# Optimization experiments

Hardware: AMD Instinct MI355X
Metric: run time of the kernel (lower is better)

The kernel has to match this reference:

```python
import jax, jax.numpy as jnp
import numpy as np

HIDDEN = 1024
NUM_HEADS = 16
HEAD_DIM = HIDDEN // NUM_HEADS


def setup_inputs() -> dict:
    key = jax.random.key(0)
    ks = jax.random.split(key, 9)
    B, S, Hs = 2, 2048, HIDDEN
    scale = 1.0 / np.sqrt(Hs)
    inp = {
        "hidden_state": jax.random.normal(ks[0], (B, S, Hs), dtype=jnp.float32),
        # causal mask, exactly (B, num_heads, S, S) as the module's assert requires
        "attention_mask": jnp.broadcast_to(
            jnp.tril(jnp.ones((S, S), dtype=bool)), (B, NUM_HEADS, S, S)
        ),
        "wq": jax.random.normal(ks[1], (Hs, Hs), dtype=jnp.float32) * scale,
        "bq": jnp.zeros((Hs,), dtype=jnp.float32),
        "wk": jax.random.normal(ks[2], (Hs, Hs), dtype=jnp.float32) * scale,
        "bk": jnp.zeros((Hs,), dtype=jnp.float32),
        "wv": jax.random.normal(ks[3], (Hs, Hs), dtype=jnp.float32) * scale,
        "bv": jnp.zeros((Hs,), dtype=jnp.float32),
        "wo": jax.random.normal(ks[4], (Hs, Hs), dtype=jnp.float32) * scale,
        "bo": jnp.zeros((Hs,), dtype=jnp.float32),
    }
    return inp


def _split_heads(x):
    B, S, _ = x.shape
    return x.reshape(B, S, NUM_HEADS, HEAD_DIM).transpose(0, 2, 1, 3)  # (B,H,S,D)


def reference(hidden_state, attention_mask, wq, bq, wk, bk, wv, bv, wo, bo):
    B, S, Hs = hidden_state.shape
    # torch nn.Linear: x @ W.T + b
    q = _split_heads(hidden_state @ wq.T + bq)
    k = _split_heads(hidden_state @ wk.T + bk)
    v = _split_heads(hidden_state @ wv.T + bv)
    scores = jnp.einsum("bhsd,bhtd->bhst", q, k) / jnp.sqrt(
        jnp.asarray(HEAD_DIM, dtype=jnp.float32)
    )
    scores = jnp.where(attention_mask, scores, -jnp.inf)
    probs = jax.nn.softmax(scores, axis=-1)
    # dropout p=0.0 (eval/deterministic) -> identity
    out = jnp.einsum("bhst,bhtd->bhsd", probs, v)
    out = out.transpose(0, 2, 1, 3).reshape(B, S, Hs)
    return out @ wo.T + bo
```

## Files before the change

kernel.cpp:

```cpp
#include <hip/hip_runtime.h>
#include <stdint.h>
#include <stddef.h>


typedef __attribute__((ext_vector_type(8))) short short8;
typedef __attribute__((ext_vector_type(4))) float f32x4;
typedef __attribute__((ext_vector_type(4))) unsigned int u32x4;
typedef __attribute__((ext_vector_type(2))) unsigned int u32x2;
typedef __attribute__((ext_vector_type(4))) unsigned short u16x4;

static __device__ __forceinline__ unsigned short f2bf(float f){
  union { float f; unsigned u; } v; v.f = f;
  unsigned r = v.u + 0x7FFFu + ((v.u >> 16) & 1u);
  return (unsigned short)(r >> 16);
}
static __device__ __forceinline__ unsigned pk2bf(float lo, float hi){
  return (unsigned)f2bf(lo) | ((unsigned)f2bf(hi) << 16);
}

static __device__ __forceinline__ void gl_lds16(const void* g, void* l){
  __builtin_amdgcn_global_load_lds((const __attribute__((address_space(1))) void*)g,
                                   (__attribute__((address_space(3))) void*)l, 16, 0, 0);
}

__global__ __launch_bounds__(256) void k_cvt_all(const float* __restrict__ X,
                                                 const float* __restrict__ w0, const float* __restrict__ w1,
                                                 const float* __restrict__ w2, const float* __restrict__ w3,
                                                 unsigned short* __restrict__ Xb,
                                                 unsigned short* __restrict__ Wb){
  int bid = blockIdx.x;
  const float* src; unsigned short* dst; int i;
  if (bid < 4096){ src = X; dst = Xb; i = bid*256 + threadIdx.x; }
  else {
    int w = (bid - 4096) >> 10;
    const float* srcs[4] = {w0,w1,w2,w3};
    src = srcs[w]; dst = Wb + (size_t)w*1048576u;
    i = ((bid - 4096) & 1023)*256 + threadIdx.x;
  }
  f32x4 x = ((const f32x4*)src)[i];
  u16x4 y = { f2bf(x[0]), f2bf(x[1]), f2bf(x[2]), f2bf(x[3]) };
  ((u16x4*)dst)[i] = y;
}

template<int MODE, int MT>
__global__ __launch_bounds__(256) void k_gemm_bt(
    const unsigned short* __restrict__ A,
    const unsigned short* __restrict__ B,
    const float* __restrict__ bias0, const float* __restrict__ bias1, const float* __restrict__ bias2,
    void* __restrict__ Cout, unsigned short* __restrict__ Vt, int N, int K)
{
  static_assert(MT==64 || MT==128, "MT");
  constexpr int I  = MT/32;
  constexpr int NA = MT/64;
  __shared__ unsigned short lds_a[MT*32];
  __shared__ unsigned short lds_b[128*32];
  const int t = threadIdx.x;
  const int lane = t & 63, wave = t >> 6;
  const int wy = wave >> 1, wx = wave & 1;
  const int m0 = blockIdx.y * MT, n0 = blockIdx.x * 128;
  const int mrow = lane & 15, quad = lane >> 4;
  const unsigned short* ga = A + (size_t)(m0 + (t>>2)) * K + (t&3)*8;
  const unsigned short* gb = B + (size_t)(n0 + (t>>2)) * K + (t&3)*8;
  char* la = (char*)lds_a + wave*1024;
  char* lb = (char*)lds_b + wave*1024;

  f32x4 acc[I][4];
  #pragma unroll
  for (int i=0;i<I;i++)
    #pragma unroll
    for (int j=0;j<4;j++) acc[i][j] = (f32x4){0.f,0.f,0.f,0.f};

  for (int k0=0;k0<K;k0+=32){
    __syncthreads();
    #pragma unroll
    for (int p=0;p<NA;p++) gl_lds16(ga + (size_t)p*64*K + k0, la + p*4096);
    #pragma unroll
    for (int p=0;p<2;p++)  gl_lds16(gb + (size_t)p*64*K + k0, lb + p*4096);
    __syncthreads();
    short8 af[I], bf[4];
    #pragma unroll
    for (int i=0;i<I;i++) af[i] = *(const short8*)(lds_a + (wy*(MT/2)+i*16+mrow)*32 + quad*8);
    #pragma unroll
    for (int j=0;j<4;j++) bf[j] = *(const short8*)(lds_b + (wx*64+j*16+mrow)*32 + quad*8);
    #pragma unroll
    for (int i=0;i<I;i++)
      #pragma unroll
      for (int j=0;j<4;j++)
        acc[i][j] = __builtin_amdgcn_mfma_f32_16x16x32_bf16(af[i], bf[j], acc[i][j], 0,0,0);
  }

  const bool vblk = (MODE==0) && (n0 >= 2048);
  #pragma unroll
  for (int j=0;j<4;j++){
    int col = n0 + wx*64 + j*16 + mrow;
    float bv;
    if (MODE==0){
      int cb = col >> 10;
      const float* bp = (cb==0)?bias0:((cb==1)?bias1:bias2);
      bv = bp[col & 1023];
    } else {
      bv = bias0[col];
    }
    #pragma unroll
    for (int i=0;i<I;i++){
      int rbase = m0 + wy*(MT/2) + i*16 + quad*4;
      if (vblk){
        int bh = (rbase >> 11) * 16 + ((col >> 6) & 15);
        unsigned short* vp = Vt + ((size_t)bh*64 + (col & 63))*2048 + (rbase & 2047);
        u32x2 wv = { pk2bf(acc[i][j][0]+bv, acc[i][j][1]+bv),
                     pk2bf(acc[i][j][2]+bv, acc[i][j][3]+bv) };
        *(u32x2*)vp = wv;
      } else {
        #pragma unroll
        for (int r=0;r<4;r++){
          float v = acc[i][j][r] + bv;
          if (MODE==1) ((float*)Cout)[(size_t)(rbase+r)*N + col] = v;
          else         ((unsigned short*)Cout)[(size_t)(rbase+r)*N + col] = f2bf(v);
        }
      }
    }
  }
}

__global__ __launch_bounds__(512, 4) void k_attn(const unsigned short* __restrict__ QKV,
                                                 const unsigned short* __restrict__ Vt,
                                                 unsigned short* __restrict__ Ctx){
  __shared__ unsigned short lds_k[2][64*72];
  __shared__ unsigned short lds_v[2][64*72];
  __shared__ unsigned short lds_p[8][16*72];
  const int t = threadIdx.x;
  const int lane = t & 63, wave = t >> 6;
  const int mrow = lane & 15, quad = lane >> 4;
  const int qh = wave >> 2;
  const int bh = blockIdx.y, b = bh >> 4, h = bh & 15;
  const int qt = (bh & 16) ? (15 - blockIdx.x) : blockIdx.x;
  const int q0 = qt * 128;
  const size_t qkvbase = (size_t)b*2048*3072 + (size_t)h*64;
  const float C1 = 0.125f * 1.44269504f;
  const float C0 = -16.f  * 1.44269504f;

  const int grow = q0 + wave*16 + mrow;
  short8 qf[2];
  {
    const unsigned short* qp = QKV + qkvbase + (size_t)grow * 3072;
    qf[0] = *(const short8*)(qp + quad*8);
    qf[1] = *(const short8*)(qp + 32 + quad*8);
  }
  float l_i = 0.f;
  f32x4 oacc[4];
  #pragma unroll
  for (int c=0;c<4;c++) oacc[c] = (f32x4){0.f,0.f,0.f,0.f};

  const int njt = 2*qt + 2;
  const int mask_jt = 2*qt + qh;
  const int skip_jt = (qh==0) ? (njt-1) : -1;
  const unsigned short* kbase = QKV + qkvbase + 1024;
  const unsigned short* vbase = Vt + (size_t)bh*64*2048;
  const int sr = t >> 3, sc = (t & 7) * 8;

  u32x4 kreg = *(const u32x4*)(kbase + (size_t)sr*3072 + sc);
  u32x4 vreg = *(const u32x4*)(vbase + (size_t)sr*2048 + sc);
  *(u32x4*)(&lds_k[0][0] + sr*72 + sc) = kreg;
  *(u32x4*)(&lds_v[0][0] + sr*72 + sc) = vreg;

  int buf = 0;
  for (int jt=0;jt<njt;jt++){
    __syncthreads();

    {
      const int pj = (jt+1 < njt) ? (jt+1)*64 : 0;
      kreg = *(const u32x4*)(kbase + (size_t)(pj+sr)*3072 + sc);
      vreg = *(const u32x4*)(vbase + (size_t)sr*2048 + pj + sc);
    }

    if (jt != skip_jt){
      const int j0 = jt*64;
      const unsigned short* lk = &lds_k[buf][0];
      const unsigned short* lv = &lds_v[buf][0];

      f32x4 sacc[4];
      #pragma unroll
      for (int jb=0;jb<4;jb++) sacc[jb] = (f32x4){0.f,0.f,0.f,0.f};
      #pragma unroll
      for (int jb=0;jb<4;jb++)
        #pragma unroll
        for (int kk=0;kk<2;kk++){
          short8 kf = *(const short8*)(lk + (jb*16+mrow)*72 + kk*32 + quad*8);
          sacc[jb] = __builtin_amdgcn_mfma_f32_16x16x32_bf16(kf, qf[kk], sacc[jb], 0,0,0);
        }

      float s[4][4];
      if (jt == mask_jt){
        #pragma unroll
        for (int jb=0;jb<4;jb++){
          int jg = j0 + jb*16 + quad*4;
          #pragma unroll
          for (int r=0;r<4;r++){
            float v = fmaf(sacc[jb][r], C1, C0);
            s[jb][r] = __builtin_amdgcn_exp2f((jg + r <= grow) ? v : -1e30f);
          }
        }
      } else {
        #pragma unroll
        for (int jb=0;jb<4;jb++)
          #pragma unroll
          for (int r=0;r<4;r++)
            s[jb][r] = __builtin_amdgcn_exp2f(fmaf(sacc[jb][r], C1, C0));
      }
      #pragma unroll
      for (int jb=0;jb<4;jb++)
        #pragma unroll
        for (int r=0;r<4;r++) l_i += s[jb][r];

      unsigned short* pp = lds_p[wave];
      #pragma unroll
      for (int jb=0;jb<4;jb++){
        u32x2 w = { pk2bf(s[jb][0], s[jb][1]), pk2bf(s[jb][2], s[jb][3]) };
        *(u32x2*)(pp + mrow*72 + jb*16 + quad*4) = w;
      }
      __asm__ volatile("s_waitcnt lgkmcnt(0)" ::: "memory");
      short8 pf[2];
      pf[0] = *(const short8*)(pp + mrow*72 + quad*8);
      pf[1] = *(const short8*)(pp + mrow*72 + 32 + quad*8);

      #pragma unroll
      for (int c=0;c<4;c++)
        #pragma unroll
        for (int kk=0;kk<2;kk++){
          short8 vf = *(const short8*)(lv + (c*16+mrow)*72 + kk*32 + quad*8);
          oacc[c] = __builtin_amdgcn_mfma_f32_16x16x32_bf16(vf, pf[kk], oacc[c], 0,0,0);
        }
    }

    *(u32x4*)(&lds_k[buf^1][0] + sr*72 + sc) = kreg;
    *(u32x4*)(&lds_v[buf^1][0] + sr*72 + sc) = vreg;
    buf ^= 1;
  }

  unsigned short* cp = Ctx + (size_t)b*2048*1024 + (size_t)h*64;
  {
    float l = l_i;
    l += __shfl_xor(l, 16);
    l += __shfl_xor(l, 32);
    float rl = 1.f / l;
    size_t rowoff = (size_t)grow * 1024;
    #pragma unroll
    for (int c=0;c<4;c++){
      u32x2 w = { pk2bf(oacc[c][0]*rl, oacc[c][1]*rl),
                  pk2bf(oacc[c][2]*rl, oacc[c][3]*rl) };
      *(u32x2*)(cp + rowoff + c*16 + quad*4) = w;
    }
  }
}

extern "C" void kernel_launch(void* const* d_in, const int* in_sizes, int n_in,
                              void* d_out, int out_size, void* d_ws, size_t ws_size,
                              hipStream_t stream){
  const float* X  = (const float*)d_in[0];
  const float* wq = (const float*)d_in[2];
  const float* bq = (const float*)d_in[3];
  const float* wk = (const float*)d_in[4];
  const float* bk = (const float*)d_in[5];
  const float* wv = (const float*)d_in[6];
  const float* bv = (const float*)d_in[7];
  const float* wo = (const float*)d_in[8];
  const float* bo = (const float*)d_in[9];

  char* ws = (char*)d_ws;
  unsigned short* Xb   = (unsigned short*)(ws);
  unsigned short* Wb   = (unsigned short*)(ws + (8u<<20));
  unsigned short* QKVb = (unsigned short*)(ws + (16u<<20));
  unsigned short* Vt   = (unsigned short*)(ws + (40u<<20));
  unsigned short* Ctxb = (unsigned short*)(ws + (48u<<20));

  k_cvt_all<<<dim3(8192), 256, 0, stream>>>(X, wq, wk, wv, wo, Xb, Wb);
  k_gemm_bt<0,128><<<dim3(24, 32), 256, 0, stream>>>(Xb, Wb, bq, bk, bv, QKVb, Vt, 3072, 1024);
  k_attn<<<dim3(16, 32), 512, 0, stream>>>(QKVb, Vt, Ctxb);
  k_gemm_bt<1,64><<<dim3(8, 64), 256, 0, stream>>>(Ctxb, Wb + 3u*1048576u, bo, bo, bo,
                                                   d_out, nullptr, 1024, 1024);
}
```

Measured before the change: 696.7 us.

## Feed P directly to 16x16x16 MFMA from registers and remap attention grid

Replaces the P round-trip through LDS (write packed bf16 probabilities, then read them back as short8 fragments) with 16x16x16 bf16 MFMAs that take the per-lane score layout directly as the B operand. This removes the per-wave P scratch LDS, an LDS wait, and the store/load traffic, at the cost of twice as many smaller MFMA instructions and narrower V fragment reads. It also flattens the attention grid to 1D with a block-id swizzle that interleaves heads and batches, likely to improve CU/XCD load balance or L2 locality for the causal workload.

```diff
diff --git a/kernel.cpp b/kernel.cpp
--- a/kernel.cpp
+++ b/kernel.cpp
@@ -4,10 +4,21 @@
 
 
 typedef __attribute__((ext_vector_type(8))) short short8;
+typedef __attribute__((ext_vector_type(4))) short bf16x4;
 typedef __attribute__((ext_vector_type(4))) float f32x4;
 typedef __attribute__((ext_vector_type(4))) unsigned int u32x4;
 typedef __attribute__((ext_vector_type(2))) unsigned int u32x2;
 typedef __attribute__((ext_vector_type(4))) unsigned short u16x4;
+
+#if __has_builtin(__builtin_amdgcn_mfma_f32_16x16x16bf16_1k)
+  #define MFMA16(a,b,c) __builtin_amdgcn_mfma_f32_16x16x16bf16_1k(a,b,c,0,0,0)
+  #define HAVE_MFMA16 1
+#elif __has_builtin(__builtin_amdgcn_mfma_f32_16x16x16_bf16)
+  #define MFMA16(a,b,c) __builtin_amdgcn_mfma_f32_16x16x16_bf16(a,b,c,0,0,0)
+  #define HAVE_MFMA16 1
+#else
+  #define HAVE_MFMA16 0
+#endif
 
 static __device__ __forceinline__ unsigned short f2bf(float f){
   union { float f; unsigned u; } v; v.f = f;
@@ -127,13 +138,18 @@
                                                  unsigned short* __restrict__ Ctx){
   __shared__ unsigned short lds_k[2][64*72];
   __shared__ unsigned short lds_v[2][64*72];
+#if !HAVE_MFMA16
   __shared__ unsigned short lds_p[8][16*72];
+#endif
   const int t = threadIdx.x;
   const int lane = t & 63, wave = t >> 6;
   const int mrow = lane & 15, quad = lane >> 4;
   const int qh = wave >> 2;
-  const int bh = blockIdx.y, b = bh >> 4, h = bh & 15;
-  const int qt = (bh & 16) ? (15 - blockIdx.x) : blockIdx.x;
+  const int bid = blockIdx.x;
+  const int bh = (bid & 7) + 8*((bid >> 3) & 3);
+  const int bx = bid >> 5;
+  const int b = bh >> 4, h = bh & 15;
+  const int qt = (bh & 16) ? (15 - bx) : bx;
   const int q0 = qt * 128;
   const size_t qkvbase = (size_t)b*2048*3072 + (size_t)h*64;
   const float C1 = 0.125f * 1.44269504f;
@@ -212,6 +228,19 @@
         #pragma unroll
         for (int r=0;r<4;r++) l_i += s[jb][r];
 
+#if HAVE_MFMA16
+      #pragma unroll
+      for (int jb=0;jb<4;jb++){
+        union { unsigned u[2]; bf16x4 s4; } pu;
+        pu.u[0] = pk2bf(s[jb][0], s[jb][1]);
+        pu.u[1] = pk2bf(s[jb][2], s[jb][3]);
+        #pragma unroll
+        for (int c=0;c<4;c++){
+          bf16x4 vfr = *(const bf16x4*)(lv + (c*16+mrow)*72 + jb*16 + quad*4);
+          oacc[c] = MFMA16(vfr, pu.s4, oacc[c]);
+        }
+      }
+#else
       unsigned short* pp = lds_p[wave];
       #pragma unroll
       for (int jb=0;jb<4;jb++){
@@ -222,7 +251,6 @@
       short8 pf[2];
       pf[0] = *(const short8*)(pp + mrow*72 + quad*8);
       pf[1] = *(const short8*)(pp + mrow*72 + 32 + quad*8);
-
       #pragma unroll
       for (int c=0;c<4;c++)
         #pragma unroll
@@ -230,6 +258,7 @@
           short8 vf = *(const short8*)(lv + (c*16+mrow)*72 + kk*32 + quad*8);
           oacc[c] = __builtin_amdgcn_mfma_f32_16x16x32_bf16(vf, pf[kk], oacc[c], 0,0,0);
         }
+#endif
     }
 
     *(u32x4*)(&lds_k[buf^1][0] + sr*72 + sc) = kreg;
@@ -275,7 +304,7 @@
 
   k_cvt_all<<<dim3(8192), 256, 0, stream>>>(X, wq, wk, wv, wo, Xb, Wb);
   k_gemm_bt<0,128><<<dim3(24, 32), 256, 0, stream>>>(Xb, Wb, bq, bk, bv, QKVb, Vt, 3072, 1024);
-  k_attn<<<dim3(16, 32), 512, 0, stream>>>(QKVb, Vt, Ctxb);
+  k_attn<<<dim3(512), 512, 0, stream>>>(QKVb, Vt, Ctxb);
   k_gemm_bt<1,64><<<dim3(8, 64), 256, 0, stream>>>(Ctxb, Wb + 3u*1048576u, bo, bo, bo,
                                                    d_out, nullptr, 1024, 1024);
 }
```

Result: no change. 704.5 us (+1.1%).
